# Kernel optimization log

Measured on AMD Instinct MI355X. Metric: run time of the kernel, lower is better.

Reference implementation:

```python
import jax, jax.numpy as jnp
import numpy as np

K, N, IN_F, OUT_F = 2, 8192, 128, 64
NEG_INF = jnp.float32(-9e15)
ADJ_DENSITY = 0.01  # ~82 neighbors/node on average


def setup_inputs() -> dict:
    key = jax.random.key(0)
    k1, k2, k3, k4 = jax.random.split(key, 4)
    x = jax.random.normal(k1, (K, N, IN_F), dtype=jnp.float32)
    # binary adjacency stored dense as float (module does torch.where(adj>0) + spmm)
    adj = (jax.random.uniform(k2, (N, N)) < ADJ_DENSITY).astype(jnp.float32)
    # xavier_uniform-style init for weight
    limit = np.sqrt(6.0 / (IN_F + OUT_F)).astype(np.float32)
    weight = jax.random.uniform(k3, (IN_F, OUT_F), minval=-limit, maxval=limit, dtype=jnp.float32)
    a = jax.random.normal(k4, (2 * OUT_F, 1), dtype=jnp.float32) * 0.1
    return {"x": x, "adj": adj, "weight": weight, "a": a}


def reference(x, adj, weight, a):
    # x: [K, N, in_f]; adj: [N, N]; weight: [in_f, out_f]; a: [2*out_f, 1]
    out_f = weight.shape[1]
    Wh = jnp.einsum('kni,io->kno', x, weight)            # [K, N, out_f]
    Wh1 = Wh @ a[:out_f]                                  # [K, N, 1]
    Wh2 = Wh @ a[out_f:]                                  # [K, N, 1]
    e = jax.nn.relu(Wh1 + jnp.swapaxes(Wh2, 1, 2))        # [K, N, N] additive attention, act=relu
    att = jnp.where(adj[None, :, :] > 0, e, NEG_INF)      # mask non-edges
    att = jax.nn.softmax(att, axis=-1)                    # row-wise softmax
    h_prime = jnp.einsum('knm,kmo->kno', att, Wh)         # attention-weighted aggregation
    out = jax.nn.relu(jnp.einsum('nm,kmo->kno', adj, h_prime))  # second (spmm) aggregation + act
    return out
```

## Files before the change

kernel.cpp:

```cpp
#include <hip/hip_runtime.h>
#include <hip/hip_fp16.h>

#define NN 8192
#define INF 128
#define OUTF 64
#define KK 2
#define NROWS (KK * NN)
#define MAXD 256
#define WH_RPB 16

typedef float floatx4 __attribute__((ext_vector_type(4)));

__global__ __launch_bounds__(256) void wh_kernel(
    const float* __restrict__ x, const float* __restrict__ weight,
    const float* __restrict__ a,
    __half* __restrict__ WhI, float* __restrict__ Wh1, float* __restrict__ W2I)
{
    __shared__ float sW[INF * OUTF];
    __shared__ float sx[WH_RPB * INF];
    int tid = threadIdx.x;
#pragma unroll
    for (int idx = tid; idx < (INF * OUTF) / 4; idx += 256)
        ((float4*)sW)[idx] = ((const float4*)weight)[idx];
    int rowBase = blockIdx.x * WH_RPB;
    const float4* xb = (const float4*)(x + (size_t)rowBase * INF);
#pragma unroll
    for (int idx = tid; idx < (WH_RPB * INF) / 4; idx += 256)
        ((float4*)sx)[idx] = xb[idx];
    __syncthreads();

    int wave = tid >> 6, lane = tid & 63;
    float a1 = a[lane], a2 = a[OUTF + lane];
    for (int r = wave; r < WH_RPB; r += 4) {
        float acc = 0.f;
#pragma unroll 16
        for (int c = 0; c < INF; ++c) acc += sx[r * INF + c] * sW[c * OUTF + lane];
        int g = rowBase + r;
        int k = g >> 13;
        int j = g & (NN - 1);
        WhI[(size_t)j * 128 + k * OUTF + lane] = __float2half(acc);
        float w1 = acc * a1, w2 = acc * a2;
#pragma unroll
        for (int off = 32; off; off >>= 1) {
            w1 += __shfl_down(w1, off);
            w2 += __shfl_down(w2, off);
        }
        if (lane == 0) { Wh1[k * NN + j] = w1; W2I[j * KK + k] = w2; }
    }
}

__global__ __launch_bounds__(256) void attn_kernel(
    const float* __restrict__ adj, const __half* __restrict__ WhI,
    const float* __restrict__ Wh1, const float* __restrict__ W2I,
    __half* __restrict__ hI, int* __restrict__ deg, int* __restrict__ nbrs)
{
    __shared__ int   s_idx[MAXD];
    __shared__ float s_p0[MAXD], s_p1[MAXD];
    __shared__ float s_r0[4], s_r1[4];
    __shared__ int   s_wcnt[4];
    __shared__ float2 s_acc[256];

    int tid = threadIdx.x;
    int i = blockIdx.x;
    int lane = tid & 63, wv = tid >> 6;

    const floatx4* row4 = (const floatx4*)(adj + (size_t)i * NN);
    floatx4 v[8];
#pragma unroll
    for (int it = 0; it < 8; ++it)
        v[it] = __builtin_nontemporal_load(&row4[tid + it * 256]);
    unsigned int msk = 0;
#pragma unroll
    for (int it = 0; it < 8; ++it) {
        if (v[it].x > 0.f) msk |= 1u << (it * 4 + 0);
        if (v[it].y > 0.f) msk |= 1u << (it * 4 + 1);
        if (v[it].z > 0.f) msk |= 1u << (it * 4 + 2);
        if (v[it].w > 0.f) msk |= 1u << (it * 4 + 3);
    }
    int cnt = __popc(msk);
    int pre = cnt;
#pragma unroll
    for (int off = 1; off < 64; off <<= 1) {
        int n = __shfl_up(pre, off);
        if (lane >= off) pre += n;
    }
    if (lane == 63) s_wcnt[wv] = pre;
    __syncthreads();
    int base = 0;
#pragma unroll
    for (int w = 0; w < 4; ++w) if (w < wv) base += s_wcnt[w];
    int d = min(s_wcnt[0] + s_wcnt[1] + s_wcnt[2] + s_wcnt[3], MAXD);
    int pos = base + pre - cnt;
    while (msk) {
        int b = __ffs(msk) - 1;
        msk &= msk - 1;
        if (pos < MAXD) s_idx[pos] = (tid + (b >> 2) * 256) * 4 + (b & 3);
        ++pos;
    }
    __syncthreads();
    if (tid == 0) deg[i] = d;
    if (tid < d) nbrs[(size_t)i * MAXD + tid] = s_idx[tid];

    float wh1_0 = Wh1[i];
    float wh1_1 = Wh1[NN + i];
    float e0 = -1e30f, e1 = -1e30f;
    if (tid < d) {
        int j = s_idx[tid];
        float2 w2 = ((const float2*)W2I)[j];
        e0 = fmaxf(wh1_0 + w2.x, 0.f);
        e1 = fmaxf(wh1_1 + w2.y, 0.f);
    }
    float m0 = e0, m1 = e1;
#pragma unroll
    for (int off = 32; off; off >>= 1) {
        m0 = fmaxf(m0, __shfl_down(m0, off));
        m1 = fmaxf(m1, __shfl_down(m1, off));
    }
    if (lane == 0) { s_r0[wv] = m0; s_r1[wv] = m1; }
    __syncthreads();
    m0 = fmaxf(fmaxf(s_r0[0], s_r0[1]), fmaxf(s_r0[2], s_r0[3]));
    m1 = fmaxf(fmaxf(s_r1[0], s_r1[1]), fmaxf(s_r1[2], s_r1[3]));
    __syncthreads();
    float p0 = 0.f, p1 = 0.f;
    if (tid < d) {
        p0 = __expf(e0 - m0);
        p1 = __expf(e1 - m1);
        s_p0[tid] = p0; s_p1[tid] = p1;
    }
    float t0 = p0, t1 = p1;
#pragma unroll
    for (int off = 32; off; off >>= 1) {
        t0 += __shfl_down(t0, off);
        t1 += __shfl_down(t1, off);
    }
    if (lane == 0) { s_r0[wv] = t0; s_r1[wv] = t1; }
    __syncthreads();
    float sum0 = s_r0[0] + s_r0[1] + s_r0[2] + s_r0[3];
    float sum1 = s_r1[0] + s_r1[1] + s_r1[2] + s_r1[3];
    float inv0 = sum0 > 0.f ? 1.f / sum0 : 0.f;
    float inv1 = sum1 > 0.f ? 1.f / sum1 : 0.f;

    int grp = tid >> 6;
    int h = tid & 63;
    const float* pk = (h & 32) ? s_p1 : s_p0;
    const __half2* Wb = (const __half2*)WhI + h;
    float2 acc = {0.f, 0.f};
    int t = grp;
    for (; t + 12 < d; t += 16) {
        int j0 = s_idx[t], j1 = s_idx[t + 4], j2 = s_idx[t + 8], j3 = s_idx[t + 12];
        float q0 = pk[t], q1 = pk[t + 4], q2 = pk[t + 8], q3 = pk[t + 12];
        float2 w0 = __half22float2(Wb[(size_t)j0 * 64]);
        float2 w1 = __half22float2(Wb[(size_t)j1 * 64]);
        float2 w2 = __half22float2(Wb[(size_t)j2 * 64]);
        float2 w3 = __half22float2(Wb[(size_t)j3 * 64]);
        acc.x += q0 * w0.x + q1 * w1.x + q2 * w2.x + q3 * w3.x;
        acc.y += q0 * w0.y + q1 * w1.y + q2 * w2.y + q3 * w3.y;
    }
    for (; t < d; t += 4) {
        int j = s_idx[t]; float q = pk[t];
        float2 w = __half22float2(Wb[(size_t)j * 64]);
        acc.x += q * w.x; acc.y += q * w.y;
    }
    s_acc[tid] = acc;
    __syncthreads();
    if (tid < 64) {
        float2 v0 = s_acc[tid], v1 = s_acc[64 + tid],
               v2 = s_acc[128 + tid], v3 = s_acc[192 + tid];
        float inv = (tid & 32) ? inv1 : inv0;
        float2 r = { (v0.x + v1.x + v2.x + v3.x) * inv,
                     (v0.y + v1.y + v2.y + v3.y) * inv };
        ((__half2*)hI)[(size_t)i * 64 + tid] = __float22half2_rn(r);
    }
}

__global__ __launch_bounds__(256) void spmm_kernel(
    const __half* __restrict__ hI, const int* __restrict__ deg,
    const int* __restrict__ nbrs, float* __restrict__ out)
{
    __shared__ int   s_idx[MAXD];
    __shared__ float2 s_acc[256];
    int tid = threadIdx.x, i = blockIdx.x;
    int d = deg[i];
    if (tid < d) s_idx[tid] = nbrs[(size_t)i * MAXD + tid];
    __syncthreads();

    int grp = tid >> 6, h = tid & 63;
    const __half2* hb = (const __half2*)hI + h;
    float2 acc = {0.f, 0.f};
    int t = grp;
    for (; t + 12 < d; t += 16) {
        int j0 = s_idx[t], j1 = s_idx[t + 4], j2 = s_idx[t + 8], j3 = s_idx[t + 12];
        float2 w0 = __half22float2(hb[(size_t)j0 * 64]);
        float2 w1 = __half22float2(hb[(size_t)j1 * 64]);
        float2 w2 = __half22float2(hb[(size_t)j2 * 64]);
        float2 w3 = __half22float2(hb[(size_t)j3 * 64]);
        acc.x += w0.x + w1.x + w2.x + w3.x;
        acc.y += w0.y + w1.y + w2.y + w3.y;
    }
    for (; t < d; t += 4) {
        float2 w = __half22float2(hb[(size_t)s_idx[t] * 64]);
        acc.x += w.x; acc.y += w.y;
    }
    s_acc[tid] = acc;
    __syncthreads();
    if (tid < 64) {
        float2 v0 = s_acc[tid], v1 = s_acc[64 + tid],
               v2 = s_acc[128 + tid], v3 = s_acc[192 + tid];
        int k = tid >> 5;
        float2 r = { fmaxf(v0.x + v1.x + v2.x + v3.x, 0.f),
                     fmaxf(v0.y + v1.y + v2.y + v3.y, 0.f) };
        ((float2*)(out + (size_t)k * NN * OUTF + (size_t)i * OUTF))[tid & 31] = r;
    }
}

extern "C" void kernel_launch(void* const* d_in, const int* in_sizes, int n_in,
                              void* d_out, int out_size, void* d_ws, size_t ws_size,
                              hipStream_t stream) {
    const float* x      = (const float*)d_in[0];
    const float* adj    = (const float*)d_in[1];
    const float* weight = (const float*)d_in[2];
    const float* a      = (const float*)d_in[3];
    float* out = (float*)d_out;

    __half* WhI = (__half*)d_ws;
    __half* hI  = WhI + (size_t)NN * 128;
    float*  Wh1 = (float*)(hI + (size_t)NN * 128);
    float*  W2I = Wh1 + NROWS;
    int*    deg = (int*)(W2I + (size_t)NN * KK);
    int*    nbrs = deg + NN;

    wh_kernel<<<NROWS / WH_RPB, 256, 0, stream>>>(x, weight, a, WhI, Wh1, W2I);
    attn_kernel<<<NN, 256, 0, stream>>>(adj, WhI, Wh1, W2I, hI, deg, nbrs);
    spmm_kernel<<<NN, 256, 0, stream>>>(hI, deg, nbrs, out);
}
```

Measured before the change: 388.3 us.

## Map one wavefront per graph row in attention and spmm kernels

Each 64-lane wavefront now processes a whole adjacency row, and each block handles four rows, replacing the block-per-row scheme. This removes block-wide __syncthreads and the shared-memory cross-wave reductions in favour of wave-local xor shuffles. The adjacency row is streamed in four chunks, with the next chunk's loads issued before the current one is processed. Gather loops are unrolled by 8 to keep more loads in flight, at the cost of more registers and a serial per-wave gather over all neighbours.

```diff
diff --git a/kernel.cpp b/kernel.cpp
--- a/kernel.cpp
+++ b/kernel.cpp
@@ -54,163 +54,152 @@
     const float* __restrict__ Wh1, const float* __restrict__ W2I,
     __half* __restrict__ hI, int* __restrict__ deg, int* __restrict__ nbrs)
 {
-    __shared__ int   s_idx[MAXD];
-    __shared__ float s_p0[MAXD], s_p1[MAXD];
-    __shared__ float s_r0[4], s_r1[4];
-    __shared__ int   s_wcnt[4];
-    __shared__ float2 s_acc[256];
-
-    int tid = threadIdx.x;
-    int i = blockIdx.x;
-    int lane = tid & 63, wv = tid >> 6;
-
+    __shared__ int   s_idx[4][MAXD];
+    __shared__ float s_p0[4][MAXD];
+    __shared__ float s_p1[4][MAXD];
+
+    int tid = threadIdx.x, lane = tid & 63, wv = tid >> 6;
+    int i = blockIdx.x * 4 + wv;
     const floatx4* row4 = (const floatx4*)(adj + (size_t)i * NN);
-    floatx4 v[8];
+
+    floatx4 vA[8], vB[8];
 #pragma unroll
     for (int it = 0; it < 8; ++it)
-        v[it] = __builtin_nontemporal_load(&row4[tid + it * 256]);
-    unsigned int msk = 0;
-#pragma unroll
-    for (int it = 0; it < 8; ++it) {
-        if (v[it].x > 0.f) msk |= 1u << (it * 4 + 0);
-        if (v[it].y > 0.f) msk |= 1u << (it * 4 + 1);
-        if (v[it].z > 0.f) msk |= 1u << (it * 4 + 2);
-        if (v[it].w > 0.f) msk |= 1u << (it * 4 + 3);
-    }
-    int cnt = __popc(msk);
-    int pre = cnt;
-#pragma unroll
-    for (int off = 1; off < 64; off <<= 1) {
-        int n = __shfl_up(pre, off);
-        if (lane >= off) pre += n;
-    }
-    if (lane == 63) s_wcnt[wv] = pre;
-    __syncthreads();
+        vA[it] = __builtin_nontemporal_load(&row4[it * 64 + lane]);
     int base = 0;
 #pragma unroll
-    for (int w = 0; w < 4; ++w) if (w < wv) base += s_wcnt[w];
-    int d = min(s_wcnt[0] + s_wcnt[1] + s_wcnt[2] + s_wcnt[3], MAXD);
-    int pos = base + pre - cnt;
-    while (msk) {
-        int b = __ffs(msk) - 1;
-        msk &= msk - 1;
-        if (pos < MAXD) s_idx[pos] = (tid + (b >> 2) * 256) * 4 + (b & 3);
-        ++pos;
-    }
-    __syncthreads();
-    if (tid == 0) deg[i] = d;
-    if (tid < d) nbrs[(size_t)i * MAXD + tid] = s_idx[tid];
-
-    float wh1_0 = Wh1[i];
-    float wh1_1 = Wh1[NN + i];
-    float e0 = -1e30f, e1 = -1e30f;
-    if (tid < d) {
-        int j = s_idx[tid];
-        float2 w2 = ((const float2*)W2I)[j];
-        e0 = fmaxf(wh1_0 + w2.x, 0.f);
-        e1 = fmaxf(wh1_1 + w2.y, 0.f);
-    }
-    float m0 = e0, m1 = e1;
+    for (int c = 0; c < 4; ++c) {
+        if (c < 3) {
+#pragma unroll
+            for (int it = 0; it < 8; ++it)
+                vB[it] = __builtin_nontemporal_load(
+                    &row4[(c + 1) * 512 + it * 64 + lane]);
+        }
+        unsigned int msk = 0;
+#pragma unroll
+        for (int it = 0; it < 8; ++it) {
+            if (vA[it].x > 0.f) msk |= 1u << (it * 4 + 0);
+            if (vA[it].y > 0.f) msk |= 1u << (it * 4 + 1);
+            if (vA[it].z > 0.f) msk |= 1u << (it * 4 + 2);
+            if (vA[it].w > 0.f) msk |= 1u << (it * 4 + 3);
+        }
+        int cnt = __popc(msk);
+        int pre = cnt;
+#pragma unroll
+        for (int off = 1; off < 64; off <<= 1) {
+            int n = __shfl_up(pre, off);
+            if (lane >= off) pre += n;
+        }
+        int tot = __shfl(pre, 63);
+        int pos = base + pre - cnt;
+        while (msk) {
+            int b = __ffs(msk) - 1;
+            msk &= msk - 1;
+            if (pos < MAXD)
+                s_idx[wv][pos] = (c * 512 + (b >> 2) * 64 + lane) * 4 + (b & 3);
+            ++pos;
+        }
+        base += tot;
+#pragma unroll
+        for (int it = 0; it < 8; ++it) vA[it] = vB[it];
+    }
+    int d = min(base, MAXD);
+    if (lane == 0) deg[i] = d;
+    for (int t = lane; t < d; t += 64) nbrs[(size_t)i * MAXD + t] = s_idx[wv][t];
+
+    float wh1_0 = Wh1[i], wh1_1 = Wh1[NN + i];
+    float e0[4], e1[4];
+    float m0 = -1e30f, m1 = -1e30f;
+#pragma unroll
+    for (int s = 0; s < 4; ++s) {
+        int t = lane + s * 64;
+        e0[s] = -1e30f; e1[s] = -1e30f;
+        if (t < d) {
+            int j = s_idx[wv][t];
+            float2 w2 = ((const float2*)W2I)[j];
+            e0[s] = fmaxf(wh1_0 + w2.x, 0.f);
+            e1[s] = fmaxf(wh1_1 + w2.y, 0.f);
+        }
+        m0 = fmaxf(m0, e0[s]); m1 = fmaxf(m1, e1[s]);
+    }
 #pragma unroll
     for (int off = 32; off; off >>= 1) {
-        m0 = fmaxf(m0, __shfl_down(m0, off));
-        m1 = fmaxf(m1, __shfl_down(m1, off));
-    }
-    if (lane == 0) { s_r0[wv] = m0; s_r1[wv] = m1; }
-    __syncthreads();
-    m0 = fmaxf(fmaxf(s_r0[0], s_r0[1]), fmaxf(s_r0[2], s_r0[3]));
-    m1 = fmaxf(fmaxf(s_r1[0], s_r1[1]), fmaxf(s_r1[2], s_r1[3]));
-    __syncthreads();
-    float p0 = 0.f, p1 = 0.f;
-    if (tid < d) {
-        p0 = __expf(e0 - m0);
-        p1 = __expf(e1 - m1);
-        s_p0[tid] = p0; s_p1[tid] = p1;
-    }
-    float t0 = p0, t1 = p1;
+        m0 = fmaxf(m0, __shfl_xor(m0, off));
+        m1 = fmaxf(m1, __shfl_xor(m1, off));
+    }
+    float sum0 = 0.f, sum1 = 0.f;
+#pragma unroll
+    for (int s = 0; s < 4; ++s) {
+        int t = lane + s * 64;
+        if (t < d) {
+            float p0 = __expf(e0[s] - m0), p1 = __expf(e1[s] - m1);
+            s_p0[wv][t] = p0; s_p1[wv][t] = p1;
+            sum0 += p0; sum1 += p1;
+        }
+    }
 #pragma unroll
     for (int off = 32; off; off >>= 1) {
-        t0 += __shfl_down(t0, off);
-        t1 += __shfl_down(t1, off);
-    }
-    if (lane == 0) { s_r0[wv] = t0; s_r1[wv] = t1; }
-    __syncthreads();
-    float sum0 = s_r0[0] + s_r0[1] + s_r0[2] + s_r0[3];
-    float sum1 = s_r1[0] + s_r1[1] + s_r1[2] + s_r1[3];
+        sum0 += __shfl_xor(sum0, off);
+        sum1 += __shfl_xor(sum1, off);
+    }
     float inv0 = sum0 > 0.f ? 1.f / sum0 : 0.f;
     float inv1 = sum1 > 0.f ? 1.f / sum1 : 0.f;
 
-    int grp = tid >> 6;
-    int h = tid & 63;
-    const float* pk = (h & 32) ? s_p1 : s_p0;
+    int h = lane;
+    const float* pk = (h & 32) ? s_p1[wv] : s_p0[wv];
     const __half2* Wb = (const __half2*)WhI + h;
     float2 acc = {0.f, 0.f};
-    int t = grp;
-    for (; t + 12 < d; t += 16) {
-        int j0 = s_idx[t], j1 = s_idx[t + 4], j2 = s_idx[t + 8], j3 = s_idx[t + 12];
-        float q0 = pk[t], q1 = pk[t + 4], q2 = pk[t + 8], q3 = pk[t + 12];
-        float2 w0 = __half22float2(Wb[(size_t)j0 * 64]);
-        float2 w1 = __half22float2(Wb[(size_t)j1 * 64]);
-        float2 w2 = __half22float2(Wb[(size_t)j2 * 64]);
-        float2 w3 = __half22float2(Wb[(size_t)j3 * 64]);
-        acc.x += q0 * w0.x + q1 * w1.x + q2 * w2.x + q3 * w3.x;
-        acc.y += q0 * w0.y + q1 * w1.y + q2 * w2.y + q3 * w3.y;
-    }
-    for (; t < d; t += 4) {
-        int j = s_idx[t]; float q = pk[t];
-        float2 w = __half22float2(Wb[(size_t)j * 64]);
+    int t = 0;
+    for (; t + 7 < d; t += 8) {
+        float2 w[8]; float q[8];
+#pragma unroll
+        for (int u = 0; u < 8; ++u) {
+            int j = s_idx[wv][t + u];
+            q[u] = pk[t + u];
+            w[u] = __half22float2(Wb[(size_t)j * 64]);
+        }
+#pragma unroll
+        for (int u = 0; u < 8; ++u) { acc.x += q[u] * w[u].x; acc.y += q[u] * w[u].y; }
+    }
+    for (; t < d; ++t) {
+        float2 w = __half22float2(Wb[(size_t)s_idx[wv][t] * 64]);
+        float q = pk[t];
         acc.x += q * w.x; acc.y += q * w.y;
     }
-    s_acc[tid] = acc;
-    __syncthreads();
-    if (tid < 64) {
-        float2 v0 = s_acc[tid], v1 = s_acc[64 + tid],
-               v2 = s_acc[128 + tid], v3 = s_acc[192 + tid];
-        float inv = (tid & 32) ? inv1 : inv0;
-        float2 r = { (v0.x + v1.x + v2.x + v3.x) * inv,
-                     (v0.y + v1.y + v2.y + v3.y) * inv };
-        ((__half2*)hI)[(size_t)i * 64 + tid] = __float22half2_rn(r);
-    }
+    float inv = (h & 32) ? inv1 : inv0;
+    float2 r = { acc.x * inv, acc.y * inv };
+    ((__half2*)hI)[(size_t)i * 64 + h] = __float22half2_rn(r);
 }
 
 __global__ __launch_bounds__(256) void spmm_kernel(
     const __half* __restrict__ hI, const int* __restrict__ deg,
     const int* __restrict__ nbrs, float* __restrict__ out)
 {
-    __shared__ int   s_idx[MAXD];
-    __shared__ float2 s_acc[256];
-    int tid = threadIdx.x, i = blockIdx.x;
+    __shared__ int s_idx[4][MAXD];
+    int tid = threadIdx.x, lane = tid & 63, wv = tid >> 6;
+    int i = blockIdx.x * 4 + wv;
     int d = deg[i];
-    if (tid < d) s_idx[tid] = nbrs[(size_t)i * MAXD + tid];
-    __syncthreads();
-
-    int grp = tid >> 6, h = tid & 63;
+    for (int t = lane; t < d; t += 64) s_idx[wv][t] = nbrs[(size_t)i * MAXD + t];
+
+    int h = lane;
     const __half2* hb = (const __half2*)hI + h;
     float2 acc = {0.f, 0.f};
-    int t = grp;
-    for (; t + 12 < d; t += 16) {
-        int j0 = s_idx[t], j1 = s_idx[t + 4], j2 = s_idx[t + 8], j3 = s_idx[t + 12];
-        float2 w0 = __half22float2(hb[(size_t)j0 * 64]);
-        float2 w1 = __half22float2(hb[(size_t)j1 * 64]);
-        float2 w2 = __half22float2(hb[(size_t)j2 * 64]);
-        float2 w3 = __half22float2(hb[(size_t)j3 * 64]);
-        acc.x += w0.x + w1.x + w2.x + w3.x;
-        acc.y += w0.y + w1.y + w2.y + w3.y;
-    }
-    for (; t < d; t += 4) {
-        float2 w = __half22float2(hb[(size_t)s_idx[t] * 64]);
+    int t = 0;
+    for (; t + 7 < d; t += 8) {
+        float2 w[8];
+#pragma unroll
+        for (int u = 0; u < 8; ++u)
+            w[u] = __half22float2(hb[(size_t)s_idx[wv][t + u] * 64]);
+#pragma unroll
+        for (int u = 0; u < 8; ++u) { acc.x += w[u].x; acc.y += w[u].y; }
+    }
+    for (; t < d; ++t) {
+        float2 w = __half22float2(hb[(size_t)s_idx[wv][t] * 64]);
         acc.x += w.x; acc.y += w.y;
     }
-    s_acc[tid] = acc;
-    __syncthreads();
-    if (tid < 64) {
-        float2 v0 = s_acc[tid], v1 = s_acc[64 + tid],
-               v2 = s_acc[128 + tid], v3 = s_acc[192 + tid];
-        int k = tid >> 5;
-        float2 r = { fmaxf(v0.x + v1.x + v2.x + v3.x, 0.f),
-                     fmaxf(v0.y + v1.y + v2.y + v3.y, 0.f) };
-        ((float2*)(out + (size_t)k * NN * OUTF + (size_t)i * OUTF))[tid & 31] = r;
-    }
+    int k = h >> 5;
+    float2 r = { fmaxf(acc.x, 0.f), fmaxf(acc.y, 0.f) };
+    ((float2*)(out + ((size_t)k * NN + i) * OUTF))[h & 31] = r;
 }
 
 extern "C" void kernel_launch(void* const* d_in, const int* in_sizes, int n_in,
@@ -230,6 +219,6 @@
     int*    nbrs = deg + NN;
 
     wh_kernel<<<NROWS / WH_RPB, 256, 0, stream>>>(x, weight, a, WhI, Wh1, W2I);
-    attn_kernel<<<NN, 256, 0, stream>>>(adj, WhI, Wh1, W2I, hI, deg, nbrs);
-    spmm_kernel<<<NN, 256, 0, stream>>>(hI, deg, nbrs, out);
-}
+    attn_kernel<<<NN / 4, 256, 0, stream>>>(adj, WhI, Wh1, W2I, hI, deg, nbrs);
+    spmm_kernel<<<NN / 4, 256, 0, stream>>>(hI, deg, nbrs, out);
+}
```

Result: no change. 385.0 us (-0.9%).
